# Kernel optimization log

Hardware: AMD Instinct MI355X
Metric: run time of the kernel (lower is better)

## Reference

```python
import jax, jax.numpy as jnp
import numpy as np


def setup_inputs() -> dict:
    key = jax.random.key(0)
    k1, k2, k3 = jax.random.split(key, 3)
    B, C, H, W = 16, 512, 64, 64
    K = 32
    std = 1.0 / (K * C) ** 0.5
    x = jax.random.normal(k1, (B, C, H, W), dtype=jnp.float32)
    codewords = jax.random.uniform(k2, (K, C), dtype=jnp.float32, minval=-std, maxval=std)
    scale = jax.random.uniform(k3, (K,), dtype=jnp.float32, minval=-1.0, maxval=0.0)
    return {"x": x, "codewords": codewords, "scale": scale}


def reference(x, codewords, scale):
    # x: [B, C, H, W] -> tokens [B, N, C] with N = H*W
    B, C, H, W = x.shape
    xf = x.reshape(B, C, H * W).transpose(0, 2, 1)  # [B, N, C]

    # (avoids materializing the [B, N, K, C] tensor the torch code builds)
    x_sq = jnp.sum(xf * xf, axis=-1)                 # [B, N]
    c_sq = jnp.sum(codewords * codewords, axis=-1)   # [K]
    xc = jnp.einsum('bnc,kc->bnk', xf, codewords)    # [B, N, K]
    scaled_l2 = scale * (x_sq[..., None] - 2.0 * xc + c_sq)  # [B, N, K]

    w = jax.nn.softmax(scaled_l2, axis=2)            # [B, N, K]

    # aggregate: sum_n w[b,n,k] * (x[b,n,:] - c[k,:])
    #          = einsum(w, x) - (sum_n w) * c
    enc = jnp.einsum('bnk,bnc->bkc', w, xf) - jnp.sum(w, axis=1)[..., None] * codewords
    return enc  # [B, K, C]
```

## Files before the change

### kernel.cpp

```cpp
#include <hip/hip_runtime.h>


#define B_ 16
#define C_ 512
#define N_ 4096
#define K_ 32
#define CWS 520
#define WLS 40

typedef __attribute__((ext_vector_type(8))) short short8;
typedef __attribute__((ext_vector_type(16))) float floatx16;

__device__ inline unsigned short f2bf(float f) {
    union { float f; unsigned u; } v; v.f = f;
    unsigned r = v.u + 0x7FFFu + ((v.u >> 16) & 1u);
    return (unsigned short)(r >> 16);
}
__device__ inline float bf2f(unsigned short s) {
    union { unsigned u; float f; } v; v.u = ((unsigned)s) << 16;
    return v.f;
}

template <int USE_WS>
__global__ __launch_bounds__(256, 2)
void enc_kernel(const float* __restrict__ x, const float* __restrict__ cw,
                const float* __restrict__ scale, float* __restrict__ outp)
{
    __shared__ unsigned short cwT[K_ * CWS];
    __shared__ unsigned short Wl[4][K_ * WLS];
    __shared__ float csq[K_];
    __shared__ float scl[K_];

    const int tid  = threadIdx.x;
    const int wave = tid >> 6;
    const int lane = tid & 63;
    const int l31  = lane & 31;
    const int lh   = lane >> 5;

    const int b     = blockIdx.x >> 5;
    const int chunk = blockIdx.x & 31;
    const float* xb = x + (long)b * C_ * N_;

    const int n0 = chunk * 128 + wave * 32;
    const float* xg = xb + n0 + l31;
    float xv[3][16];
#define G1LOAD(st_, sp_)                                                       \
    { _Pragma("unroll")                                                        \
      for (int u = 0; u < 16; ++u)                                             \
          xv[st_][u] = xg[(long)((sp_) * 32 + (u >> 3) * 16 + lh * 8 + (u & 7)) * N_]; }
    G1LOAD(0, 0)
    G1LOAD(1, 1)
    G1LOAD(2, 2)

    if (tid < K_) scl[tid] = scale[tid];
    {
        const int k = tid >> 3, p = tid & 7;
        const float4* src = (const float4*)(cw + k * C_ + p * 64);
        float s = 0.f;
        #pragma unroll
        for (int i = 0; i < 16; ++i) {
            const float4 v = src[i];
            s += v.x*v.x + v.y*v.y + v.z*v.z + v.w*v.w;
            const unsigned lo = (unsigned)f2bf(v.x) | ((unsigned)f2bf(v.y) << 16);
            const unsigned hi = (unsigned)f2bf(v.z) | ((unsigned)f2bf(v.w) << 16);
            *(uint2*)&cwT[k * CWS + p * 64 + i * 4] = make_uint2(lo, hi);
        }
        s += __shfl_xor(s, 1); s += __shfl_xor(s, 2); s += __shfl_xor(s, 4);
        if (p == 0) csq[k] = s;
    }
    __syncthreads();

    floatx16 S;
    #pragma unroll
    for (int i = 0; i < 16; ++i) S[i] = 0.f;
    float xsq = 0.f;

    #pragma unroll
    for (int sp = 0; sp < 16; ++sp) {
        const int st = sp % 3;
        #pragma unroll
        for (int h = 0; h < 2; ++h) {
            const int s = sp * 2 + h;
            const short8 af = *(const short8*)&cwT[l31 * CWS + s * 16 + lh * 8];
            short8 bx;
            #pragma unroll
            for (int j = 0; j < 8; ++j) {
                const float v = xv[st][h * 8 + j];
                xsq += v * v;
                bx[j] = (short)f2bf(v);
            }
            S = __builtin_amdgcn_mfma_f32_32x32x16_bf16(af, bx, S, 0, 0, 0);
        }
        if (sp + 3 < 16) G1LOAD(st, sp + 3)
    }
    xsq += __shfl_xor(xsq, 32);

    {
        float L[16], mx = -3.4e38f;
        #pragma unroll
        for (int r = 0; r < 16; ++r) {
            const int k = (r & 3) + 8 * (r >> 2) + 4 * lh;
            L[r] = scl[k] * (xsq - 2.f * S[r] + csq[k]);
            mx = fmaxf(mx, L[r]);
        }
        mx = fmaxf(mx, __shfl_xor(mx, 32));
        float sum = 0.f;
        #pragma unroll
        for (int r = 0; r < 16; ++r) { L[r] = __expf(L[r] - mx); sum += L[r]; }
        sum += __shfl_xor(sum, 32);
        const float inv = 1.f / sum;
        #pragma unroll
        for (int r = 0; r < 16; ++r) {
            const int k = (r & 3) + 8 * (r >> 2) + 4 * lh;
            Wl[wave][k * WLS + l31] = f2bf(L[r] * inv);
        }
    }

    float4 bv[6][2];
#define G2LOAD(bi_, i_)                                                        \
    { const int t_ = (i_) >> 3, st_ = (i_) & 7;                                \
      const int c_ = wave * 128 + t_ * 32 + l31;                               \
      const int no_ = (st_ >> 1) * 32 + (st_ & 1) * 16 + lh * 8;               \
      const float* p_ = xb + (long)c_ * N_ + chunk * 128 + no_;                \
      bv[bi_][0] = *(const float4*)p_;                                         \
      bv[bi_][1] = *(const float4*)(p_ + 4); }
    G2LOAD(0, 0)
    G2LOAD(1, 1)
    G2LOAD(2, 2)
    G2LOAD(3, 3)
    G2LOAD(4, 4)
    G2LOAD(5, 5)

    __syncthreads();

    short8 aw[8];
    #pragma unroll
    for (int st = 0; st < 8; ++st)
        aw[st] = *(const short8*)&Wl[st >> 1][l31 * WLS + (st & 1) * 16 + lh * 8];

    floatx16 wacc;
    #pragma unroll
    for (int i = 0; i < 16; ++i) wacc[i] = 0.f;
    {
        short8 ones;
        #pragma unroll
        for (int j = 0; j < 8; ++j) ones[j] = (short)0x3F80;
        #pragma unroll
        for (int st = 0; st < 8; ++st)
            wacc = __builtin_amdgcn_mfma_f32_32x32x16_bf16(aw[st], ones, wacc, 0, 0, 0);
    }

    floatx16 acc[4];
    #pragma unroll
    for (int t = 0; t < 4; ++t)
        #pragma unroll
        for (int i = 0; i < 16; ++i) acc[t][i] = 0.f;

    #pragma unroll
    for (int i = 0; i < 32; ++i) {
        const int bi = i % 6;
        const int t  = i >> 3, st = i & 7;
        const float4 v0 = bv[bi][0];
        const float4 v1 = bv[bi][1];
        short8 bx;
        bx[0] = (short)f2bf(v0.x); bx[1] = (short)f2bf(v0.y);
        bx[2] = (short)f2bf(v0.z); bx[3] = (short)f2bf(v0.w);
        bx[4] = (short)f2bf(v1.x); bx[5] = (short)f2bf(v1.y);
        bx[6] = (short)f2bf(v1.z); bx[7] = (short)f2bf(v1.w);
        acc[t] = __builtin_amdgcn_mfma_f32_32x32x16_bf16(aw[st], bx, acc[t], 0, 0, 0);
        if (i + 6 < 32) G2LOAD(bi, i + 6)
    }

    float* dst = USE_WS ? (outp + (size_t)blockIdx.x * K_ * C_)
                        : (outp + (size_t)b * K_ * C_);
    #pragma unroll
    for (int t = 0; t < 4; ++t) {
        const int c = wave * 128 + t * 32 + l31;
        #pragma unroll
        for (int r = 0; r < 16; ++r) {
            const int k = (r & 3) + 8 * (r >> 2) + 4 * lh;
            const float cwv = bf2f(cwT[k * CWS + c]);
            const float val = acc[t][r] - wacc[r] * cwv;
            if (USE_WS) dst[k * C_ + c] = val;
            else        atomicAdd(dst + k * C_ + c, val);
        }
    }
}

__global__ __launch_bounds__(256)
void reduce_kernel(const float4* __restrict__ part, float4* __restrict__ out)
{
    const int gid = blockIdx.x * 256 + threadIdx.x;
    const int bb  = gid >> 12;
    const int i4  = gid & 4095;
    const float4* p = part + ((size_t)bb * 32) * 4096 + i4;
    float4 s = make_float4(0.f, 0.f, 0.f, 0.f);
    #pragma unroll
    for (int ch = 0; ch < 32; ++ch) {
        const float4 v = p[(size_t)ch * 4096];
        s.x += v.x; s.y += v.y; s.z += v.z; s.w += v.w;
    }
    out[gid] = s;
}

extern "C" void kernel_launch(void* const* d_in, const int* in_sizes, int n_in,
                              void* d_out, int out_size, void* d_ws, size_t ws_size,
                              hipStream_t stream) {
    const float* x     = (const float*)d_in[0];
    const float* cw    = (const float*)d_in[1];
    const float* scale = (const float*)d_in[2];
    float* out = (float*)d_out;

    const size_t ws_need = (size_t)512 * K_ * C_ * sizeof(float);
    if (ws_size >= ws_need) {
        float* part = (float*)d_ws;
        hipLaunchKernelGGL(enc_kernel<1>, dim3(B_ * 32), dim3(256), 0, stream,
                           x, cw, scale, part);
        hipLaunchKernelGGL(reduce_kernel, dim3(256), dim3(256), 0, stream,
                           (const float4*)part, (float4*)out);
    } else {
        hipMemsetAsync(out, 0, (size_t)out_size * sizeof(float), stream);
        hipLaunchKernelGGL(enc_kernel<0>, dim3(B_ * 32), dim3(256), 0, stream,
                           x, cw, scale, out);
    }
}
```

Measured before the change: 217.0 us.

## Stage x tile through LDS with coalesced float4 loads and double buffering

Phase 1 used to load x with scalar per-lane loads strided by N, one channel per load. It now loads whole 128-token rows as coalesced float4 chunks, converts them to bf16 and writes them into a double-buffered LDS tile that the MFMA operands read from. The per-token squared norm is now accumulated as partial sums across threads and reduced through shared memory. This is meant to cut global memory transactions in the first GEMM, at the cost of more LDS traffic, extra barriers per stage and more shared memory, which may lower occupancy.

```diff
diff --git a/kernel.cpp b/kernel.cpp
--- a/kernel.cpp
+++ b/kernel.cpp
@@ -7,6 +7,7 @@
 #define K_ 32
 #define CWS 520
 #define WLS 40
+#define XCP 132
 
 typedef __attribute__((ext_vector_type(8))) short short8;
 typedef __attribute__((ext_vector_type(16))) float floatx16;
@@ -27,7 +28,9 @@
                 const float* __restrict__ scale, float* __restrict__ outp)
 {
     __shared__ unsigned short cwT[K_ * CWS];
+    __shared__ unsigned short XC[2][64 * XCP];
     __shared__ unsigned short Wl[4][K_ * WLS];
+    __shared__ float xsqp[4][128];
     __shared__ float csq[K_];
     __shared__ float scl[K_];
 
@@ -41,21 +44,35 @@
     const int chunk = blockIdx.x & 31;
     const float* xb = x + (long)b * C_ * N_;
 
-    const int n0 = chunk * 128 + wave * 32;
-    const float* xg = xb + n0 + l31;
-    float xv[3][16];
-#define G1LOAD(st_, sp_)                                                       \
+    const int r = tid >> 5;
+    const int p = tid & 31;
+    const float* xrow = xb + chunk * 128 + p * 4;
+
+    float4 sA[8], sB[8];
+#define XISSUE(buf_, g_)                                                       \
     { _Pragma("unroll")                                                        \
-      for (int u = 0; u < 16; ++u)                                             \
-          xv[st_][u] = xg[(long)((sp_) * 32 + (u >> 3) * 16 + lh * 8 + (u & 7)) * N_]; }
-    G1LOAD(0, 0)
-    G1LOAD(1, 1)
-    G1LOAD(2, 2)
+      for (int i = 0; i < 8; ++i)                                              \
+          buf_[i] = *(const float4*)(xrow + (long)((g_) * 64 + i * 8 + r) * N_); }
+
+    float xs0 = 0.f, xs1 = 0.f, xs2 = 0.f, xs3 = 0.f;
+#define XWRITE(buf_, dst_)                                                     \
+    { _Pragma("unroll")                                                        \
+      for (int i = 0; i < 8; ++i) {                                            \
+          const float4 v = buf_[i];                                            \
+          xs0 += v.x * v.x; xs1 += v.y * v.y;                                  \
+          xs2 += v.z * v.z; xs3 += v.w * v.w;                                  \
+          const unsigned lo = (unsigned)f2bf(v.x) | ((unsigned)f2bf(v.y) << 16);\
+          const unsigned hi = (unsigned)f2bf(v.z) | ((unsigned)f2bf(v.w) << 16);\
+          *(uint2*)&XC[dst_][(i * 8 + r) * XCP + p * 4] = make_uint2(lo, hi);  \
+      } }
+
+    XISSUE(sA, 0)
+    XISSUE(sB, 1)
 
     if (tid < K_) scl[tid] = scale[tid];
     {
-        const int k = tid >> 3, p = tid & 7;
-        const float4* src = (const float4*)(cw + k * C_ + p * 64);
+        const int k = tid >> 3, q = tid & 7;
+        const float4* src = (const float4*)(cw + k * C_ + q * 64);
         float s = 0.f;
         #pragma unroll
         for (int i = 0; i < 16; ++i) {
@@ -63,57 +80,44 @@
             s += v.x*v.x + v.y*v.y + v.z*v.z + v.w*v.w;
             const unsigned lo = (unsigned)f2bf(v.x) | ((unsigned)f2bf(v.y) << 16);
             const unsigned hi = (unsigned)f2bf(v.z) | ((unsigned)f2bf(v.w) << 16);
-            *(uint2*)&cwT[k * CWS + p * 64 + i * 4] = make_uint2(lo, hi);
+            *(uint2*)&cwT[k * CWS + q * 64 + i * 4] = make_uint2(lo, hi);
         }
         s += __shfl_xor(s, 1); s += __shfl_xor(s, 2); s += __shfl_xor(s, 4);
-        if (p == 0) csq[k] = s;
-    }
+        if (q == 0) csq[k] = s;
+    }
+
+    XWRITE(sA, 0)
     __syncthreads();
 
     floatx16 S;
     #pragma unroll
     for (int i = 0; i < 16; ++i) S[i] = 0.f;
-    float xsq = 0.f;
-
-    #pragma unroll
-    for (int sp = 0; sp < 16; ++sp) {
-        const int st = sp % 3;
-        #pragma unroll
-        for (int h = 0; h < 2; ++h) {
-            const int s = sp * 2 + h;
-            const short8 af = *(const short8*)&cwT[l31 * CWS + s * 16 + lh * 8];
+
+    #pragma unroll
+    for (int g = 0; g < 8; ++g) {
+        if (g + 2 < 8) {
+            if ((g & 1) == 0) { XISSUE(sA, g + 2) } else { XISSUE(sB, g + 2) }
+        }
+        #pragma unroll
+        for (int s = 0; s < 4; ++s) {
+            const short8 af = *(const short8*)&cwT[l31 * CWS + (g * 4 + s) * 16 + lh * 8];
             short8 bx;
             #pragma unroll
-            for (int j = 0; j < 8; ++j) {
-                const float v = xv[st][h * 8 + j];
-                xsq += v * v;
-                bx[j] = (short)f2bf(v);
-            }
+            for (int j = 0; j < 8; ++j)
+                bx[j] = (short)XC[g & 1][(s * 16 + lh * 8 + j) * XCP + wave * 32 + l31];
             S = __builtin_amdgcn_mfma_f32_32x32x16_bf16(af, bx, S, 0, 0, 0);
         }
-        if (sp + 3 < 16) G1LOAD(st, sp + 3)
-    }
-    xsq += __shfl_xor(xsq, 32);
-
-    {
-        float L[16], mx = -3.4e38f;
-        #pragma unroll
-        for (int r = 0; r < 16; ++r) {
-            const int k = (r & 3) + 8 * (r >> 2) + 4 * lh;
-            L[r] = scl[k] * (xsq - 2.f * S[r] + csq[k]);
-            mx = fmaxf(mx, L[r]);
-        }
-        mx = fmaxf(mx, __shfl_xor(mx, 32));
-        float sum = 0.f;
-        #pragma unroll
-        for (int r = 0; r < 16; ++r) { L[r] = __expf(L[r] - mx); sum += L[r]; }
-        sum += __shfl_xor(sum, 32);
-        const float inv = 1.f / sum;
-        #pragma unroll
-        for (int r = 0; r < 16; ++r) {
-            const int k = (r & 3) + 8 * (r >> 2) + 4 * lh;
-            Wl[wave][k * WLS + l31] = f2bf(L[r] * inv);
-        }
+        if (g + 1 < 8) {
+            if ((g & 1) == 0) { XWRITE(sB, (g + 1) & 1) } else { XWRITE(sA, (g + 1) & 1) }
+        }
+        if (g < 7) __syncthreads();
+    }
+
+    xs0 += __shfl_xor(xs0, 32); xs1 += __shfl_xor(xs1, 32);
+    xs2 += __shfl_xor(xs2, 32); xs3 += __shfl_xor(xs3, 32);
+    if (lane < 32) {
+        xsqp[wave][l31 * 4 + 0] = xs0; xsqp[wave][l31 * 4 + 1] = xs1;
+        xsqp[wave][l31 * 4 + 2] = xs2; xsqp[wave][l31 * 4 + 3] = xs3;
     }
 
     float4 bv[6][2];
@@ -133,6 +137,30 @@
 
     __syncthreads();
 
+    {
+        const int n = wave * 32 + l31;
+        const float xq = xsqp[0][n] + xsqp[1][n] + xsqp[2][n] + xsqp[3][n];
+        float L[16], mx = -3.4e38f;
+        #pragma unroll
+        for (int rr = 0; rr < 16; ++rr) {
+            const int k = (rr & 3) + 8 * (rr >> 2) + 4 * lh;
+            L[rr] = scl[k] * (xq - 2.f * S[rr] + csq[k]);
+            mx = fmaxf(mx, L[rr]);
+        }
+        mx = fmaxf(mx, __shfl_xor(mx, 32));
+        float sum = 0.f;
+        #pragma unroll
+        for (int rr = 0; rr < 16; ++rr) { L[rr] = __expf(L[rr] - mx); sum += L[rr]; }
+        sum += __shfl_xor(sum, 32);
+        const float inv = 1.f / sum;
+        #pragma unroll
+        for (int rr = 0; rr < 16; ++rr) {
+            const int k = (rr & 3) + 8 * (rr >> 2) + 4 * lh;
+            Wl[wave][k * WLS + l31] = f2bf(L[rr] * inv);
+        }
+    }
+    __syncthreads();
+
     short8 aw[8];
     #pragma unroll
     for (int st = 0; st < 8; ++st)
@@ -177,10 +205,10 @@
     for (int t = 0; t < 4; ++t) {
         const int c = wave * 128 + t * 32 + l31;
         #pragma unroll
-        for (int r = 0; r < 16; ++r) {
-            const int k = (r & 3) + 8 * (r >> 2) + 4 * lh;
+        for (int rr = 0; rr < 16; ++rr) {
+            const int k = (rr & 3) + 8 * (rr >> 2) + 4 * lh;
             const float cwv = bf2f(cwT[k * CWS + c]);
-            const float val = acc[t][r] - wacc[r] * cwv;
+            const float val = acc[t][rr] - wacc[rr] * cwv;
             if (USE_WS) dst[k * C_ + c] = val;
             else        atomicAdd(dst + k * C_ + c, val);
         }
```

Measured after the change: 216.1 us. Within noise of the previous version (-0.4%).

## Halve token chunk per block, split channel reduction across wave pairs

Applied to the files above, without the earlier changes.

Each block now covers 64 tokens instead of 128, giving 1024 blocks. Pairs of waves split the 512 channels of the distance GEMM and combine partial scores through shared-memory atomics before the softmax. Codeword fragments now sit in registers instead of a bf16 shared-memory transpose, which cuts shared memory and allows 4 blocks per CU. The cost is twice as many partial outputs for the reduce kernel to read, extra shared atomics and a sync, and only half the waves doing the softmax.

```diff
diff --git a/kernel.cpp b/kernel.cpp
--- a/kernel.cpp
+++ b/kernel.cpp
@@ -5,7 +5,6 @@
 #define C_ 512
 #define N_ 4096
 #define K_ 32
-#define CWS 520
 #define WLS 40
 
 typedef __attribute__((ext_vector_type(8))) short short8;
@@ -16,18 +15,15 @@
     unsigned r = v.u + 0x7FFFu + ((v.u >> 16) & 1u);
     return (unsigned short)(r >> 16);
 }
-__device__ inline float bf2f(unsigned short s) {
-    union { unsigned u; float f; } v; v.u = ((unsigned)s) << 16;
-    return v.f;
-}
 
 template <int USE_WS>
-__global__ __launch_bounds__(256, 2)
+__global__ __launch_bounds__(256, 4)
 void enc_kernel(const float* __restrict__ x, const float* __restrict__ cw,
                 const float* __restrict__ scale, float* __restrict__ outp)
 {
-    __shared__ unsigned short cwT[K_ * CWS];
-    __shared__ unsigned short Wl[4][K_ * WLS];
+    __shared__ float Sred[2][32][33];
+    __shared__ unsigned short Wl[2][K_ * WLS];
+    __shared__ float xsqp[4][32];
     __shared__ float csq[K_];
     __shared__ float scl[K_];
 
@@ -37,36 +33,48 @@
     const int l31  = lane & 31;
     const int lh   = lane >> 5;
 
-    const int b     = blockIdx.x >> 5;
-    const int chunk = blockIdx.x & 31;
+    const int b     = blockIdx.x >> 6;
+    const int chunk = blockIdx.x & 63;
+    const int g     = wave >> 1;
+    const int coff  = (wave & 1) * 256;
     const float* xb = x + (long)b * C_ * N_;
 
-    const int n0 = chunk * 128 + wave * 32;
+    const int n0 = chunk * 64 + g * 32;
     const float* xg = xb + n0 + l31;
     float xv[3][16];
 #define G1LOAD(st_, sp_)                                                       \
     { _Pragma("unroll")                                                        \
       for (int u = 0; u < 16; ++u)                                             \
-          xv[st_][u] = xg[(long)((sp_) * 32 + (u >> 3) * 16 + lh * 8 + (u & 7)) * N_]; }
+          xv[st_][u] = xg[(long)(coff + (sp_) * 32 + (u >> 3) * 16             \
+                                 + lh * 8 + (u & 7)) * N_]; }
     G1LOAD(0, 0)
     G1LOAD(1, 1)
     G1LOAD(2, 2)
 
+    short8 af[16];
+    #pragma unroll
+    for (int s = 0; s < 16; ++s) {
+        const float4 a0 = *(const float4*)(cw + l31 * C_ + coff + s * 16 + lh * 8);
+        const float4 a1 = *(const float4*)(cw + l31 * C_ + coff + s * 16 + lh * 8 + 4);
+        af[s][0] = (short)f2bf(a0.x); af[s][1] = (short)f2bf(a0.y);
+        af[s][2] = (short)f2bf(a0.z); af[s][3] = (short)f2bf(a0.w);
+        af[s][4] = (short)f2bf(a1.x); af[s][5] = (short)f2bf(a1.y);
+        af[s][6] = (short)f2bf(a1.z); af[s][7] = (short)f2bf(a1.w);
+    }
+
     if (tid < K_) scl[tid] = scale[tid];
+    for (int i = tid; i < 2 * 32 * 33; i += 256) ((float*)Sred)[i] = 0.f;
     {
-        const int k = tid >> 3, p = tid & 7;
-        const float4* src = (const float4*)(cw + k * C_ + p * 64);
+        const int k = tid >> 3, q = tid & 7;
+        const float4* src = (const float4*)(cw + k * C_ + q * 64);
         float s = 0.f;
         #pragma unroll
         for (int i = 0; i < 16; ++i) {
             const float4 v = src[i];
             s += v.x*v.x + v.y*v.y + v.z*v.z + v.w*v.w;
-            const unsigned lo = (unsigned)f2bf(v.x) | ((unsigned)f2bf(v.y) << 16);
-            const unsigned hi = (unsigned)f2bf(v.z) | ((unsigned)f2bf(v.w) << 16);
-            *(uint2*)&cwT[k * CWS + p * 64 + i * 4] = make_uint2(lo, hi);
         }
         s += __shfl_xor(s, 1); s += __shfl_xor(s, 2); s += __shfl_xor(s, 4);
-        if (p == 0) csq[k] = s;
+        if (q == 0) csq[k] = s;
     }
     __syncthreads();
 
@@ -76,12 +84,11 @@
     float xsq = 0.f;
 
     #pragma unroll
-    for (int sp = 0; sp < 16; ++sp) {
+    for (int sp = 0; sp < 8; ++sp) {
         const int st = sp % 3;
         #pragma unroll
         for (int h = 0; h < 2; ++h) {
             const int s = sp * 2 + h;
-            const short8 af = *(const short8*)&cwT[l31 * CWS + s * 16 + lh * 8];
             short8 bx;
             #pragma unroll
             for (int j = 0; j < 8; ++j) {
@@ -89,18 +96,27 @@
                 xsq += v * v;
                 bx[j] = (short)f2bf(v);
             }
-            S = __builtin_amdgcn_mfma_f32_32x32x16_bf16(af, bx, S, 0, 0, 0);
-        }
-        if (sp + 3 < 16) G1LOAD(st, sp + 3)
+            S = __builtin_amdgcn_mfma_f32_32x32x16_bf16(af[s], bx, S, 0, 0, 0);
+        }
+        if (sp + 3 < 8) G1LOAD(st, sp + 3)
     }
     xsq += __shfl_xor(xsq, 32);
-
-    {
+    if (lh == 0) xsqp[wave][l31] = xsq;
+
+    #pragma unroll
+    for (int r = 0; r < 16; ++r) {
+        const int k = (r & 3) + 8 * (r >> 2) + 4 * lh;
+        atomicAdd(&Sred[g][l31][k], S[r]);
+    }
+    __syncthreads();
+
+    if ((wave & 1) == 0) {
+        const float xq = xsqp[wave][l31] + xsqp[wave + 1][l31];
         float L[16], mx = -3.4e38f;
         #pragma unroll
         for (int r = 0; r < 16; ++r) {
             const int k = (r & 3) + 8 * (r >> 2) + 4 * lh;
-            L[r] = scl[k] * (xsq - 2.f * S[r] + csq[k]);
+            L[r] = scl[k] * (xq - 2.f * Sred[g][l31][k] + csq[k]);
             mx = fmaxf(mx, L[r]);
         }
         mx = fmaxf(mx, __shfl_xor(mx, 32));
@@ -112,30 +128,27 @@
         #pragma unroll
         for (int r = 0; r < 16; ++r) {
             const int k = (r & 3) + 8 * (r >> 2) + 4 * lh;
-            Wl[wave][k * WLS + l31] = f2bf(L[r] * inv);
-        }
-    }
-
-    float4 bv[6][2];
+            Wl[g][k * WLS + l31] = f2bf(L[r] * inv);
+        }
+    }
+
+    float4 bv[3][2];
 #define G2LOAD(bi_, i_)                                                        \
-    { const int t_ = (i_) >> 3, st_ = (i_) & 7;                                \
+    { const int t_ = (i_) >> 2, st_ = (i_) & 3;                                \
       const int c_ = wave * 128 + t_ * 32 + l31;                               \
       const int no_ = (st_ >> 1) * 32 + (st_ & 1) * 16 + lh * 8;               \
-      const float* p_ = xb + (long)c_ * N_ + chunk * 128 + no_;                \
+      const float* p_ = xb + (long)c_ * N_ + chunk * 64 + no_;                 \
       bv[bi_][0] = *(const float4*)p_;                                         \
       bv[bi_][1] = *(const float4*)(p_ + 4); }
     G2LOAD(0, 0)
     G2LOAD(1, 1)
     G2LOAD(2, 2)
-    G2LOAD(3, 3)
-    G2LOAD(4, 4)
-    G2LOAD(5, 5)
 
     __syncthreads();
 
-    short8 aw[8];
-    #pragma unroll
-    for (int st = 0; st < 8; ++st)
+    short8 aw[4];
+    #pragma unroll
+    for (int st = 0; st < 4; ++st)
         aw[st] = *(const short8*)&Wl[st >> 1][l31 * WLS + (st & 1) * 16 + lh * 8];
 
     floatx16 wacc;
@@ -146,7 +159,7 @@
         #pragma unroll
         for (int j = 0; j < 8; ++j) ones[j] = (short)0x3F80;
         #pragma unroll
-        for (int st = 0; st < 8; ++st)
+        for (int st = 0; st < 4; ++st)
             wacc = __builtin_amdgcn_mfma_f32_32x32x16_bf16(aw[st], ones, wacc, 0, 0, 0);
     }
 
@@ -157,9 +170,9 @@
         for (int i = 0; i < 16; ++i) acc[t][i] = 0.f;
 
     #pragma unroll
-    for (int i = 0; i < 32; ++i) {
-        const int bi = i % 6;
-        const int t  = i >> 3, st = i & 7;
+    for (int i = 0; i < 16; ++i) {
+        const int bi = i % 3;
+        const int t  = i >> 2, st = i & 3;
         const float4 v0 = bv[bi][0];
         const float4 v1 = bv[bi][1];
         short8 bx;
@@ -168,7 +181,7 @@
         bx[4] = (short)f2bf(v1.x); bx[5] = (short)f2bf(v1.y);
         bx[6] = (short)f2bf(v1.z); bx[7] = (short)f2bf(v1.w);
         acc[t] = __builtin_amdgcn_mfma_f32_32x32x16_bf16(aw[st], bx, acc[t], 0, 0, 0);
-        if (i + 6 < 32) G2LOAD(bi, i + 6)
+        if (i + 3 < 16) G2LOAD(bi, i + 3)
     }
 
     float* dst = USE_WS ? (outp + (size_t)blockIdx.x * K_ * C_)
@@ -179,8 +192,7 @@
         #pragma unroll
         for (int r = 0; r < 16; ++r) {
             const int k = (r & 3) + 8 * (r >> 2) + 4 * lh;
-            const float cwv = bf2f(cwT[k * CWS + c]);
-            const float val = acc[t][r] - wacc[r] * cwv;
+            const float val = acc[t][r] - wacc[r] * cw[k * C_ + c];
             if (USE_WS) dst[k * C_ + c] = val;
             else        atomicAdd(dst + k * C_ + c, val);
         }
@@ -193,10 +205,10 @@
     const int gid = blockIdx.x * 256 + threadIdx.x;
     const int bb  = gid >> 12;
     const int i4  = gid & 4095;
-    const float4* p = part + ((size_t)bb * 32) * 4096 + i4;
+    const float4* p = part + ((size_t)bb * 64) * 4096 + i4;
     float4 s = make_float4(0.f, 0.f, 0.f, 0.f);
     #pragma unroll
-    for (int ch = 0; ch < 32; ++ch) {
+    for (int ch = 0; ch < 64; ++ch) {
         const float4 v = p[(size_t)ch * 4096];
         s.x += v.x; s.y += v.y; s.z += v.z; s.w += v.w;
     }
@@ -211,16 +223,16 @@
     const float* scale = (const float*)d_in[2];
     float* out = (float*)d_out;
 
-    const size_t ws_need = (size_t)512 * K_ * C_ * sizeof(float);
+    const size_t ws_need = (size_t)1024 * K_ * C_ * sizeof(float);
     if (ws_size >= ws_need) {
         float* part = (float*)d_ws;
-        hipLaunchKernelGGL(enc_kernel<1>, dim3(B_ * 32), dim3(256), 0, stream,
+        hipLaunchKernelGGL(enc_kernel<1>, dim3(1024), dim3(256), 0, stream,
                            x, cw, scale, part);
         hipLaunchKernelGGL(reduce_kernel, dim3(256), dim3(256), 0, stream,
                            (const float4*)part, (float4*)out);
     } else {
         hipMemsetAsync(out, 0, (size_t)out_size * sizeof(float), stream);
-        hipLaunchKernelGGL(enc_kernel<0>, dim3(B_ * 32), dim3(256), 0, stream,
+        hipLaunchKernelGGL(enc_kernel<0>, dim3(1024), dim3(256), 0, stream,
                            x, cw, scale, out);
     }
 }
```

Measured after the change: 331.5 us. 1.53x slower.
